# Performance work log

Hardware: AMD Instinct MI355X
Metric: run time of the kernel (lower is better)

Reference implementation:

```python
import jax, jax.numpy as jnp
import numpy as np

CELL = 1024
IN = 1024
HYB = 1024
SPK = 256
B = 8192

def setup_inputs() -> dict:
    key = jax.random.key(0)
    ks = jax.random.split(key, 13)
    s = lambda fan: 1.0 / np.sqrt(fan)
    return {
        "x": jax.random.normal(ks[0], (B, IN), jnp.float32),
        "ctm": jax.random.normal(ks[1], (B, CELL), jnp.float32),
        "htm": jax.random.normal(ks[2], (B, CELL), jnp.float32),
        "ztm": jax.random.normal(ks[3], (B, HYB), jnp.float32),
        "speaker_affine": jax.random.normal(ks[4], (B, SPK), jnp.float32),
        "Ww": jax.random.uniform(ks[5], (IN, 4 * CELL), jnp.float32, -s(IN), s(IN)),
        "Wb": jax.random.uniform(ks[6], (4 * CELL,), jnp.float32, -s(IN), s(IN)),
        "Uw": jax.random.uniform(ks[7], (CELL, 4 * CELL), jnp.float32, -s(CELL), s(CELL)),
        "Ub": jax.random.uniform(ks[8], (4 * CELL,), jnp.float32, -s(CELL), s(CELL)),
        "Vw": jax.random.uniform(ks[9], (HYB, CELL), jnp.float32, -s(HYB), s(HYB)),
        "Vb": jax.random.uniform(ks[10], (CELL,), jnp.float32, -s(HYB), s(HYB)),
        "Sw": jax.random.uniform(ks[11], (SPK, 4 * CELL), jnp.float32, -s(SPK), s(SPK)),
        "Sb": jax.random.uniform(ks[12], (4 * CELL,), jnp.float32, -s(SPK), s(SPK)),
    }

def reference(x, ctm, htm, ztm, speaker_affine, Ww, Wb, Uw, Ub, Vw, Vb, Sw, Sb):
    # sums: [B, 4*CELL] = W(x) + U(htm) + S(speaker)
    sums = (x @ Ww + Wb) + (htm @ Uw + Ub) + (speaker_affine @ Sw + Sb)
    hybrid = ztm @ Vw + Vb  # [B, CELL]
    f_t = jax.nn.sigmoid(sums[:, :CELL])
    i_t = jax.nn.sigmoid(sums[:, CELL:2 * CELL])
    o_t = jax.nn.sigmoid(sums[:, 2 * CELL:3 * CELL])
    ch_t = jnp.tanh(sums[:, 3 * CELL:])
    f_t_ = jax.nn.sigmoid(hybrid)
    c_t = f_t * ctm + i_t * ch_t + f_t_ * ctm
    h_t = jnp.tanh(c_t) * o_t
    return (c_t, h_t)
```

## Files before the change

kernel.cpp:

```cpp
#include <hip/hip_runtime.h>

#define B_DIM 8192
#define CELL  1024
#define KA    3328
#define NSUM  5120
#define BM    256
#define BN    256
#define BK    64

typedef unsigned short u16;
typedef __attribute__((ext_vector_type(8))) short bf16x8;
typedef __attribute__((ext_vector_type(4))) float f32x4;
typedef __attribute__((ext_vector_type(4))) float fx4;
typedef __attribute__((ext_vector_type(4))) unsigned short u16x4;

__device__ inline u16 f2bf(float f) {
  unsigned u = __float_as_uint(f);
  return (u16)((u + 0x7FFFu + ((u >> 16) & 1u)) >> 16);
}
__device__ inline float bf2f(u16 h) { return __uint_as_float(((unsigned)h) << 16); }
__device__ inline float sigmoidf(float v) { return 1.0f / (1.0f + __expf(-v)); }

__global__ void cvt_cat(const float* __restrict__ src, u16* __restrict__ dst,
                        int shift, int colOff, int n4) {
  int i = blockIdx.x * 256 + threadIdx.x;
  if (i >= n4) return;
  int e = i << 2;
  int row = e >> shift;
  int col = e & ((1 << shift) - 1);
  float4 v = *reinterpret_cast<const float4*>(src + e);
  u16x4 o;
  o[0] = f2bf(v.x); o[1] = f2bf(v.y); o[2] = f2bf(v.z); o[3] = f2bf(v.w);
  *reinterpret_cast<u16x4*>(dst + (size_t)row * KA + colOff + col) = o;
}

__global__ void wtrans(const float* __restrict__ src, int N,
                       u16* __restrict__ dst, int KT, int koff) {
  __shared__ float tile[32][33];
  int n0 = blockIdx.x * 32, k0 = blockIdx.y * 32;
  int tx = threadIdx.x, ty = threadIdx.y;
#pragma unroll
  for (int j = 0; j < 4; ++j)
    tile[ty + j * 8][tx] = src[(size_t)(k0 + ty + j * 8) * N + n0 + tx];
  __syncthreads();
#pragma unroll
  for (int j = 0; j < 4; ++j)
    dst[(size_t)(n0 + ty + j * 8) * KT + koff + k0 + tx] = f2bf(tile[tx][ty + j * 8]);
}

__device__ __forceinline__ void gload_lds16(const void* g, void* l) {
  __builtin_amdgcn_global_load_lds((const __attribute__((address_space(1))) void*)g,
                                   (__attribute__((address_space(3))) void*)l,
                                   16, 0, 0);
}

__device__ __forceinline__ void stage_half(const u16* __restrict__ g0, int ldk,
                                           u16* ldsTile, int half, int kt,
                                           int wave, int lane) {
#pragma unroll
  for (int k2 = 0; k2 < 2; ++k2) {
    const int r0 = half * 128 + k2 * 64 + wave * 8;
    const int r = r0 + (lane >> 3);
    const int slot = (lane & 7) ^ (lane >> 3);
    const u16* g = g0 + (size_t)r * ldk + kt * 64 + slot * 8;
    gload_lds16((const void*)g, (void*)(ldsTile + r0 * 64));
  }
}

#define LD_A(ASP, QP)                                                              \
  aq[0][0] = *reinterpret_cast<const bf16x8*>((ASP) + aBase0 + (2 * (QP)) * 1024);     \
  aq[0][1] = *reinterpret_cast<const bf16x8*>((ASP) + aBase1 + (2 * (QP)) * 1024);     \
  aq[1][0] = *reinterpret_cast<const bf16x8*>((ASP) + aBase0 + (2 * (QP) + 1) * 1024); \
  aq[1][1] = *reinterpret_cast<const bf16x8*>((ASP) + aBase1 + (2 * (QP) + 1) * 1024);

#define LD_B(BSP)                                                                  \
  _Pragma("unroll")                                                                \
  for (int n = 0; n < 4; ++n) {                                                    \
    br[n][0] = *reinterpret_cast<const bf16x8*>((BSP) + bBase0 + n * 1024);        \
    br[n][1] = *reinterpret_cast<const bf16x8*>((BSP) + bBase1 + n * 1024);        \
  }

#define MFMA_PH(QP)                                                                \
  __builtin_amdgcn_s_setprio(1);                                                   \
  _Pragma("unroll")                                                                \
  for (int q = 0; q < 2; ++q) {                                                    \
    _Pragma("unroll")                                                              \
    for (int n = 0; n < 4; ++n) {                                                  \
      acc[2 * (QP) + q][n] = __builtin_amdgcn_mfma_f32_16x16x32_bf16(              \
          aq[q][0], br[n][0], acc[2 * (QP) + q][n], 0, 0, 0);                      \
      acc[2 * (QP) + q][n] = __builtin_amdgcn_mfma_f32_16x16x32_bf16(              \
          aq[q][1], br[n][1], acc[2 * (QP) + q][n], 0, 0, 0);                      \
    }                                                                              \
  }                                                                                \
  __builtin_amdgcn_s_setprio(0);

#define ENTRY_BAR                                                                  \
  __builtin_amdgcn_sched_barrier(0);                                               \
  __builtin_amdgcn_s_barrier();                                                    \
  asm volatile("s_waitcnt lgkmcnt(0)" ::: "memory");                               \
  __builtin_amdgcn_sched_barrier(0);

#define EXIT_BAR __builtin_amdgcn_s_barrier();

__global__ __launch_bounds__(512, 2) void gemm8(
    const u16* __restrict__ Afull, const u16* __restrict__ WT4a,
    const u16* __restrict__ WTVa, u16* __restrict__ sums) {
  __shared__ u16 As[2][BM * BK];
  __shared__ u16 Bs[2][BN * BK];
  const int tid = threadIdx.x;
  const int wave = tid >> 6, lane = tid & 63;
  const int wm = wave >> 2, wn = wave & 3;
  const int lrow = lane & 15, khi = lane >> 4;

  const int bx = blockIdx.x, by = blockIdx.y;
  const u16* Bsrc; int KT, nk, ncol0, aoff, nbase;
  if (bx < 16) { Bsrc = WT4a; KT = 2304; nk = 36; nbase = bx * 256; ncol0 = bx * 256; aoff = 0; }
  else         { Bsrc = WTVa; KT = 1024; nk = 16; nbase = (bx - 16) * 256; ncol0 = 4096 + (bx - 16) * 256; aoff = 2304; }
  const int m0 = by * 256;
  const u16* Ag = Afull + (size_t)m0 * KA + aoff;
  const u16* Bg = Bsrc + (size_t)nbase * KT;

  const int sw = lane & 7;
  const int swz0 = ((0 + khi) ^ sw) * 8;
  const int swz1 = ((4 + khi) ^ sw) * 8;
  const int aBase0 = (wm * 128 + lrow) * 64 + swz0;
  const int aBase1 = (wm * 128 + lrow) * 64 + swz1;
  const int bBase0 = (wn * 64 + lrow) * 64 + swz0;
  const int bBase1 = (wn * 64 + lrow) * 64 + swz1;

  f32x4 acc[8][4];
#pragma unroll
  for (int m2 = 0; m2 < 8; ++m2)
#pragma unroll
    for (int n2 = 0; n2 < 4; ++n2) acc[m2][n2] = (f32x4){0.f, 0.f, 0.f, 0.f};
  bf16x8 aq[2][2], br[4][2];
  u16* As0 = As[0]; u16* As1 = As[1]; u16* Bs0 = Bs[0]; u16* Bs1 = Bs[1];

  stage_half(Ag, KA, As0, 0, 0, wave, lane);
  stage_half(Ag, KA, As0, 1, 0, wave, lane);
  stage_half(Bg, KT, Bs0, 0, 0, wave, lane);
  stage_half(Bg, KT, Bs0, 1, 0, wave, lane);
  stage_half(Bg, KT, Bs1, 0, 1, wave, lane);
  stage_half(Bg, KT, Bs1, 1, 1, wave, lane);
  asm volatile("s_waitcnt vmcnt(4)" ::: "memory");
  __builtin_amdgcn_s_barrier();

  const int niter = nk >> 1;
  for (int it = 0; it < niter; ++it) {
    const int t = it * 2;
    const bool nl = (t + 2 < nk);
    LD_B(Bs0)
    LD_A(As0, 0)
    stage_half(Ag, KA, As1, 0, t + 1, wave, lane);
    ENTRY_BAR MFMA_PH(0) EXIT_BAR

    LD_A(As0, 1)
    stage_half(Ag, KA, As1, 1, t + 1, wave, lane);
    ENTRY_BAR MFMA_PH(1) EXIT_BAR

    LD_A(As0, 2)
    if (nl) stage_half(Bg, KT, Bs0, 0, t + 2, wave, lane);
    ENTRY_BAR MFMA_PH(2) EXIT_BAR

    LD_A(As0, 3)
    if (nl) stage_half(Bg, KT, Bs0, 1, t + 2, wave, lane);
    ENTRY_BAR MFMA_PH(3)
    if (nl) { asm volatile("s_waitcnt vmcnt(4)" ::: "memory"); }
    else    { asm volatile("s_waitcnt vmcnt(0)" ::: "memory"); }
    EXIT_BAR

    LD_B(Bs1)
    LD_A(As1, 0)
    if (nl) stage_half(Ag, KA, As0, 0, t + 2, wave, lane);
    ENTRY_BAR MFMA_PH(0) EXIT_BAR

    LD_A(As1, 1)
    if (nl) stage_half(Ag, KA, As0, 1, t + 2, wave, lane);
    ENTRY_BAR MFMA_PH(1) EXIT_BAR

    LD_A(As1, 2)
    if (nl) stage_half(Bg, KT, Bs1, 0, t + 3, wave, lane);
    ENTRY_BAR MFMA_PH(2) EXIT_BAR

    LD_A(As1, 3)
    if (nl) stage_half(Bg, KT, Bs1, 1, t + 3, wave, lane);
    ENTRY_BAR MFMA_PH(3)
    if (nl) { asm volatile("s_waitcnt vmcnt(4)" ::: "memory"); }
    else    { asm volatile("s_waitcnt vmcnt(0)" ::: "memory"); }
    EXIT_BAR
  }

#pragma unroll
  for (int mf = 0; mf < 8; ++mf) {
    const int rbase = m0 + wm * 128 + mf * 16 + khi * 4;
#pragma unroll
    for (int nf = 0; nf < 4; ++nf) {
      const int col = ncol0 + wn * 64 + nf * 16 + lrow;
#pragma unroll
      for (int j = 0; j < 4; ++j)
        sums[(size_t)(rbase + j) * NSUM + col] = f2bf(acc[mf][nf][j]);
    }
  }
}

__global__ void epilogue(const u16* __restrict__ sums, const float* __restrict__ ctm,
                         const float* __restrict__ Wb, const float* __restrict__ Ub,
                         const float* __restrict__ Sb, const float* __restrict__ Vb,
                         float* __restrict__ outC, float* __restrict__ outH) {
  int t = blockIdx.x * 256 + threadIdx.x;
  int row = t >> 8;
  int c4 = (t & 255) << 2;
  const u16* s = sums + (size_t)row * NSUM;
  u16x4 sf = *reinterpret_cast<const u16x4*>(s + c4);
  u16x4 si = *reinterpret_cast<const u16x4*>(s + 1024 + c4);
  u16x4 so = *reinterpret_cast<const u16x4*>(s + 2048 + c4);
  u16x4 sc = *reinterpret_cast<const u16x4*>(s + 3072 + c4);
  u16x4 sh = *reinterpret_cast<const u16x4*>(s + 4096 + c4);
  fx4 ct = *reinterpret_cast<const fx4*>(ctm + (size_t)row * CELL + c4);
  fx4 bF = *reinterpret_cast<const fx4*>(Wb + c4) +
           *reinterpret_cast<const fx4*>(Ub + c4) +
           *reinterpret_cast<const fx4*>(Sb + c4);
  fx4 bI = *reinterpret_cast<const fx4*>(Wb + 1024 + c4) +
           *reinterpret_cast<const fx4*>(Ub + 1024 + c4) +
           *reinterpret_cast<const fx4*>(Sb + 1024 + c4);
  fx4 bO = *reinterpret_cast<const fx4*>(Wb + 2048 + c4) +
           *reinterpret_cast<const fx4*>(Ub + 2048 + c4) +
           *reinterpret_cast<const fx4*>(Sb + 2048 + c4);
  fx4 bC = *reinterpret_cast<const fx4*>(Wb + 3072 + c4) +
           *reinterpret_cast<const fx4*>(Ub + 3072 + c4) +
           *reinterpret_cast<const fx4*>(Sb + 3072 + c4);
  fx4 bH = *reinterpret_cast<const fx4*>(Vb + c4);

  fx4 vc, vh;
#pragma unroll
  for (int j = 0; j < 4; ++j) {
    float f_ = sigmoidf(bf2f(sf[j]) + bF[j]);
    float i_ = sigmoidf(bf2f(si[j]) + bI[j]);
    float o_ = sigmoidf(bf2f(so[j]) + bO[j]);
    float g_ = tanhf(bf2f(sc[j]) + bC[j]);
    float fh = sigmoidf(bf2f(sh[j]) + bH[j]);
    float cc = (f_ + fh) * ct[j] + i_ * g_;
    vc[j] = cc;
    vh[j] = tanhf(cc) * o_;
  }
  *reinterpret_cast<fx4*>(outC + (size_t)row * CELL + c4) = vc;
  *reinterpret_cast<fx4*>(outH + (size_t)row * CELL + c4) = vh;
}

extern "C" void kernel_launch(void* const* d_in, const int* in_sizes, int n_in,
                              void* d_out, int out_size, void* d_ws, size_t ws_size,
                              hipStream_t stream) {
  const float* x   = (const float*)d_in[0];
  const float* ctm = (const float*)d_in[1];
  const float* htm = (const float*)d_in[2];
  const float* ztm = (const float*)d_in[3];
  const float* spk = (const float*)d_in[4];
  const float* Ww  = (const float*)d_in[5];
  const float* Wb  = (const float*)d_in[6];
  const float* Uw  = (const float*)d_in[7];
  const float* Ub  = (const float*)d_in[8];
  const float* Vw  = (const float*)d_in[9];
  const float* Vb  = (const float*)d_in[10];
  const float* Sw  = (const float*)d_in[11];
  const float* Sb  = (const float*)d_in[12];

  u16* Afull = (u16*)d_ws;
  u16* WT4a  = Afull + (size_t)B_DIM * KA;
  u16* WTVa  = WT4a + (size_t)4096 * 2304;
  u16* sums  = WTVa + (size_t)1024 * 1024;
  float* outC = (float*)d_out;
  float* outH = outC + (size_t)B_DIM * CELL;

  cvt_cat<<<8192, 256, 0, stream>>>(x,   Afull, 10, 0,    2097152);
  cvt_cat<<<8192, 256, 0, stream>>>(htm, Afull, 10, 1024, 2097152);
  cvt_cat<<<2048, 256, 0, stream>>>(spk, Afull, 8,  2048, 524288);
  cvt_cat<<<8192, 256, 0, stream>>>(ztm, Afull, 10, 2304, 2097152);

  wtrans<<<dim3(128, 32), dim3(32, 8), 0, stream>>>(Ww, 4096, WT4a, 2304, 0);
  wtrans<<<dim3(128, 32), dim3(32, 8), 0, stream>>>(Uw, 4096, WT4a, 2304, 1024);
  wtrans<<<dim3(128, 8),  dim3(32, 8), 0, stream>>>(Sw, 4096, WT4a, 2304, 2048);
  wtrans<<<dim3(32, 32),  dim3(32, 8), 0, stream>>>(Vw, 1024, WTVa, 1024, 0);

  gemm8<<<dim3(20, 32), 512, 0, stream>>>(Afull, WT4a, WTVa, sums);

  epilogue<<<8192, 256, 0, stream>>>(sums, ctm, Wb, Ub, Sb, Vb, outC, outH);
}
```

Before: 295.5 us.

## Fuse LSTM epilogue into GEMM via gate-interleaved weight layout

```diff
diff --git a/kernel.cpp b/kernel.cpp
--- a/kernel.cpp
+++ b/kernel.cpp
@@ -3,7 +3,6 @@
 #define B_DIM 8192
 #define CELL  1024
 #define KA    3328
-#define NSUM  5120
 #define BM    256
 #define BN    256
 #define BK    64
@@ -18,7 +17,6 @@
   unsigned u = __float_as_uint(f);
   return (u16)((u + 0x7FFFu + ((u >> 16) & 1u)) >> 16);
 }
-__device__ inline float bf2f(u16 h) { return __uint_as_float(((unsigned)h) << 16); }
 __device__ inline float sigmoidf(float v) { return 1.0f / (1.0f + __expf(-v)); }
 
 __global__ void cvt_cat(const float* __restrict__ src, u16* __restrict__ dst,
@@ -35,7 +33,7 @@
 }
 
 __global__ void wtrans(const float* __restrict__ src, int N,
-                       u16* __restrict__ dst, int KT, int koff) {
+                       u16* __restrict__ dst, int KT, int koff, int packed) {
   __shared__ float tile[32][33];
   int n0 = blockIdx.x * 32, k0 = blockIdx.y * 32;
   int tx = threadIdx.x, ty = threadIdx.y;
@@ -44,8 +42,11 @@
     tile[ty + j * 8][tx] = src[(size_t)(k0 + ty + j * 8) * N + n0 + tx];
   __syncthreads();
 #pragma unroll
-  for (int j = 0; j < 4; ++j)
-    dst[(size_t)(n0 + ty + j * 8) * KT + koff + k0 + tx] = f2bf(tile[tx][ty + j * 8]);
+  for (int j = 0; j < 4; ++j) {
+    int jj = n0 + ty + j * 8;
+    int p = packed ? (((jj & 1023) >> 4) << 6) + ((jj >> 10) << 4) + (jj & 15) : jj;
+    dst[(size_t)p * KT + koff + k0 + tx] = f2bf(tile[tx][ty + j * 8]);
+  }
 }
 
 __device__ __forceinline__ void gload_lds16(const void* g, void* l) {
@@ -102,9 +103,12 @@
 
 #define EXIT_BAR __builtin_amdgcn_s_barrier();
 
-__global__ __launch_bounds__(512, 2) void gemm8(
-    const u16* __restrict__ Afull, const u16* __restrict__ WT4a,
-    const u16* __restrict__ WTVa, u16* __restrict__ sums) {
+__global__ __launch_bounds__(512, 2) void gemm_fused(
+    const u16* __restrict__ Afull, const u16* __restrict__ WT4p,
+    const u16* __restrict__ VwT, const float* __restrict__ ctm,
+    const float* __restrict__ Wb, const float* __restrict__ Ub,
+    const float* __restrict__ Sb, const float* __restrict__ Vb,
+    float* __restrict__ outC, float* __restrict__ outH) {
   __shared__ u16 As[2][BM * BK];
   __shared__ u16 Bs[2][BN * BK];
   const int tid = threadIdx.x;
@@ -112,13 +116,13 @@
   const int wm = wave >> 2, wn = wave & 3;
   const int lrow = lane & 15, khi = lane >> 4;
 
-  const int bx = blockIdx.x, by = blockIdx.y;
-  const u16* Bsrc; int KT, nk, ncol0, aoff, nbase;
-  if (bx < 16) { Bsrc = WT4a; KT = 2304; nk = 36; nbase = bx * 256; ncol0 = bx * 256; aoff = 0; }
-  else         { Bsrc = WTVa; KT = 1024; nk = 16; nbase = (bx - 16) * 256; ncol0 = 4096 + (bx - 16) * 256; aoff = 2304; }
-  const int m0 = by * 256;
-  const u16* Ag = Afull + (size_t)m0 * KA + aoff;
-  const u16* Bg = Bsrc + (size_t)nbase * KT;
+  const int bid = blockIdx.x;
+  const int tilei = ((bid & 7) << 6) | (bid >> 3);
+  const int nb = tilei >> 5, mb = tilei & 31;
+  const int m0 = mb * 256;
+  const u16* Ag = Afull + (size_t)m0 * KA;
+  const u16* Ah = Afull + (size_t)m0 * KA + 2304;
+  const u16* Bg = WT4p + (size_t)(nb * 256) * 2304;
 
   const int sw = lane & 7;
   const int swz0 = ((0 + khi) ^ sw) * 8;
@@ -128,6 +132,9 @@
   const int bBase0 = (wn * 64 + lrow) * 64 + swz0;
   const int bBase1 = (wn * 64 + lrow) * 64 + swz1;
 
+  const int co = nb * 64 + wn * 16 + lrow;
+  const u16* HgRow = VwT + (size_t)co * 1024;
+
   f32x4 acc[8][4];
 #pragma unroll
   for (int m2 = 0; m2 < 8; ++m2)
@@ -138,17 +145,17 @@
 
   stage_half(Ag, KA, As0, 0, 0, wave, lane);
   stage_half(Ag, KA, As0, 1, 0, wave, lane);
-  stage_half(Bg, KT, Bs0, 0, 0, wave, lane);
-  stage_half(Bg, KT, Bs0, 1, 0, wave, lane);
-  stage_half(Bg, KT, Bs1, 0, 1, wave, lane);
-  stage_half(Bg, KT, Bs1, 1, 1, wave, lane);
+  stage_half(Bg, 2304, Bs0, 0, 0, wave, lane);
+  stage_half(Bg, 2304, Bs0, 1, 0, wave, lane);
+  stage_half(Bg, 2304, Bs1, 0, 1, wave, lane);
+  stage_half(Bg, 2304, Bs1, 1, 1, wave, lane);
   asm volatile("s_waitcnt vmcnt(4)" ::: "memory");
   __builtin_amdgcn_s_barrier();
 
-  const int niter = nk >> 1;
-  for (int it = 0; it < niter; ++it) {
+#pragma unroll 1
+  for (int it = 0; it < 18; ++it) {
     const int t = it * 2;
-    const bool nl = (t + 2 < nk);
+    const bool nl = (t + 2 < 36);
     LD_B(Bs0)
     LD_A(As0, 0)
     stage_half(Ag, KA, As1, 0, t + 1, wave, lane);
@@ -159,11 +166,11 @@
     ENTRY_BAR MFMA_PH(1) EXIT_BAR
 
     LD_A(As0, 2)
-    if (nl) stage_half(Bg, KT, Bs0, 0, t + 2, wave, lane);
+    if (nl) stage_half(Bg, 2304, Bs0, 0, t + 2, wave, lane);
     ENTRY_BAR MFMA_PH(2) EXIT_BAR
 
     LD_A(As0, 3)
-    if (nl) stage_half(Bg, KT, Bs0, 1, t + 2, wave, lane);
+    if (nl) stage_half(Bg, 2304, Bs0, 1, t + 2, wave, lane);
     ENTRY_BAR MFMA_PH(3)
     if (nl) { asm volatile("s_waitcnt vmcnt(4)" ::: "memory"); }
     else    { asm volatile("s_waitcnt vmcnt(0)" ::: "memory"); }
@@ -179,72 +186,61 @@
     ENTRY_BAR MFMA_PH(1) EXIT_BAR
 
     LD_A(As1, 2)
-    if (nl) stage_half(Bg, KT, Bs1, 0, t + 3, wave, lane);
+    if (nl) stage_half(Bg, 2304, Bs1, 0, t + 3, wave, lane);
     ENTRY_BAR MFMA_PH(2) EXIT_BAR
 
     LD_A(As1, 3)
-    if (nl) stage_half(Bg, KT, Bs1, 1, t + 3, wave, lane);
+    if (nl) stage_half(Bg, 2304, Bs1, 1, t + 3, wave, lane);
     ENTRY_BAR MFMA_PH(3)
     if (nl) { asm volatile("s_waitcnt vmcnt(4)" ::: "memory"); }
     else    { asm volatile("s_waitcnt vmcnt(0)" ::: "memory"); }
     EXIT_BAR
   }
 
+  f32x4 acch[8];
+#pragma unroll
+  for (int m2 = 0; m2 < 8; ++m2) acch[m2] = (f32x4){0.f, 0.f, 0.f, 0.f};
+
+#pragma unroll 1
+  for (int kt = 0; kt < 16; ++kt) {
+    __syncthreads();
+    stage_half(Ah, KA, As0, 0, kt, wave, lane);
+    stage_half(Ah, KA, As0, 1, kt, wave, lane);
+    __syncthreads();
+    bf16x8 bh0 = *reinterpret_cast<const bf16x8*>(HgRow + kt * 64 + khi * 8);
+    bf16x8 bh1 = *reinterpret_cast<const bf16x8*>(HgRow + kt * 64 + 32 + khi * 8);
+#pragma unroll
+    for (int qp = 0; qp < 4; ++qp) {
+      LD_A(As0, qp)
+      acch[2 * qp]     = __builtin_amdgcn_mfma_f32_16x16x32_bf16(aq[0][0], bh0, acch[2 * qp], 0, 0, 0);
+      acch[2 * qp]     = __builtin_amdgcn_mfma_f32_16x16x32_bf16(aq[0][1], bh1, acch[2 * qp], 0, 0, 0);
+      acch[2 * qp + 1] = __builtin_amdgcn_mfma_f32_16x16x32_bf16(aq[1][0], bh0, acch[2 * qp + 1], 0, 0, 0);
+      acch[2 * qp + 1] = __builtin_amdgcn_mfma_f32_16x16x32_bf16(aq[1][1], bh1, acch[2 * qp + 1], 0, 0, 0);
+    }
+  }
+
+  const float bf = Wb[co] + Ub[co] + Sb[co];
+  const float bi = Wb[1024 + co] + Ub[1024 + co] + Sb[1024 + co];
+  const float bo = Wb[2048 + co] + Ub[2048 + co] + Sb[2048 + co];
+  const float bc = Wb[3072 + co] + Ub[3072 + co] + Sb[3072 + co];
+  const float bv = Vb[co];
 #pragma unroll
   for (int mf = 0; mf < 8; ++mf) {
-    const int rbase = m0 + wm * 128 + mf * 16 + khi * 4;
-#pragma unroll
-    for (int nf = 0; nf < 4; ++nf) {
-      const int col = ncol0 + wn * 64 + nf * 16 + lrow;
-#pragma unroll
-      for (int j = 0; j < 4; ++j)
-        sums[(size_t)(rbase + j) * NSUM + col] = f2bf(acc[mf][nf][j]);
+    const int r0 = m0 + wm * 128 + mf * 16 + khi * 4;
+#pragma unroll
+    for (int j = 0; j < 4; ++j) {
+      const size_t idx = (size_t)(r0 + j) * CELL + co;
+      float f_ = sigmoidf(acc[mf][0][j] + bf);
+      float i_ = sigmoidf(acc[mf][1][j] + bi);
+      float o_ = sigmoidf(acc[mf][2][j] + bo);
+      float g_ = tanhf(acc[mf][3][j] + bc);
+      float fh = sigmoidf(acch[mf][j] + bv);
+      float ct = ctm[idx];
+      float cc = (f_ + fh) * ct + i_ * g_;
+      outC[idx] = cc;
+      outH[idx] = tanhf(cc) * o_;
     }
   }
-}
-
-__global__ void epilogue(const u16* __restrict__ sums, const float* __restrict__ ctm,
-                         const float* __restrict__ Wb, const float* __restrict__ Ub,
-                         const float* __restrict__ Sb, const float* __restrict__ Vb,
-                         float* __restrict__ outC, float* __restrict__ outH) {
-  int t = blockIdx.x * 256 + threadIdx.x;
-  int row = t >> 8;
-  int c4 = (t & 255) << 2;
-  const u16* s = sums + (size_t)row * NSUM;
-  u16x4 sf = *reinterpret_cast<const u16x4*>(s + c4);
-  u16x4 si = *reinterpret_cast<const u16x4*>(s + 1024 + c4);
-  u16x4 so = *reinterpret_cast<const u16x4*>(s + 2048 + c4);
-  u16x4 sc = *reinterpret_cast<const u16x4*>(s + 3072 + c4);
-  u16x4 sh = *reinterpret_cast<const u16x4*>(s + 4096 + c4);
-  fx4 ct = *reinterpret_cast<const fx4*>(ctm + (size_t)row * CELL + c4);
-  fx4 bF = *reinterpret_cast<const fx4*>(Wb + c4) +
-           *reinterpret_cast<const fx4*>(Ub + c4) +
-           *reinterpret_cast<const fx4*>(Sb + c4);
-  fx4 bI = *reinterpret_cast<const fx4*>(Wb + 1024 + c4) +
-           *reinterpret_cast<const fx4*>(Ub + 1024 + c4) +
-           *reinterpret_cast<const fx4*>(Sb + 1024 + c4);
-  fx4 bO = *reinterpret_cast<const fx4*>(Wb + 2048 + c4) +
-           *reinterpret_cast<const fx4*>(Ub + 2048 + c4) +
-           *reinterpret_cast<const fx4*>(Sb + 2048 + c4);
-  fx4 bC = *reinterpret_cast<const fx4*>(Wb + 3072 + c4) +
-           *reinterpret_cast<const fx4*>(Ub + 3072 + c4) +
-           *reinterpret_cast<const fx4*>(Sb + 3072 + c4);
-  fx4 bH = *reinterpret_cast<const fx4*>(Vb + c4);
-
-  fx4 vc, vh;
-#pragma unroll
-  for (int j = 0; j < 4; ++j) {
-    float f_ = sigmoidf(bf2f(sf[j]) + bF[j]);
-    float i_ = sigmoidf(bf2f(si[j]) + bI[j]);
-    float o_ = sigmoidf(bf2f(so[j]) + bO[j]);
-    float g_ = tanhf(bf2f(sc[j]) + bC[j]);
-    float fh = sigmoidf(bf2f(sh[j]) + bH[j]);
-    float cc = (f_ + fh) * ct[j] + i_ * g_;
-    vc[j] = cc;
-    vh[j] = tanhf(cc) * o_;
-  }
-  *reinterpret_cast<fx4*>(outC + (size_t)row * CELL + c4) = vc;
-  *reinterpret_cast<fx4*>(outH + (size_t)row * CELL + c4) = vh;
 }
 
 extern "C" void kernel_launch(void* const* d_in, const int* in_sizes, int n_in,
@@ -265,9 +261,8 @@
   const float* Sb  = (const float*)d_in[12];
 
   u16* Afull = (u16*)d_ws;
-  u16* WT4a  = Afull + (size_t)B_DIM * KA;
-  u16* WTVa  = WT4a + (size_t)4096 * 2304;
-  u16* sums  = WTVa + (size_t)1024 * 1024;
+  u16* WT4p  = Afull + (size_t)B_DIM * KA;
+  u16* VwT   = WT4p + (size_t)4096 * 2304;
   float* outC = (float*)d_out;
   float* outH = outC + (size_t)B_DIM * CELL;
 
@@ -276,12 +271,10 @@
   cvt_cat<<<2048, 256, 0, stream>>>(spk, Afull, 8,  2048, 524288);
   cvt_cat<<<8192, 256, 0, stream>>>(ztm, Afull, 10, 2304, 2097152);
 
-  wtrans<<<dim3(128, 32), dim3(32, 8), 0, stream>>>(Ww, 4096, WT4a, 2304, 0);
-  wtrans<<<dim3(128, 32), dim3(32, 8), 0, stream>>>(Uw, 4096, WT4a, 2304, 1024);
-  wtrans<<<dim3(128, 8),  dim3(32, 8), 0, stream>>>(Sw, 4096, WT4a, 2304, 2048);
-  wtrans<<<dim3(32, 32),  dim3(32, 8), 0, stream>>>(Vw, 1024, WTVa, 1024, 0);
-
-  gemm8<<<dim3(20, 32), 512, 0, stream>>>(Afull, WT4a, WTVa, sums);
-
-  epilogue<<<8192, 256, 0, stream>>>(sums, ctm, Wb, Ub, Sb, Vb, outC, outH);
-}
+  wtrans<<<dim3(128, 32), dim3(32, 8), 0, stream>>>(Ww, 4096, WT4p, 2304, 0,    1);
+  wtrans<<<dim3(128, 32), dim3(32, 8), 0, stream>>>(Uw, 4096, WT4p, 2304, 1024, 1);
+  wtrans<<<dim3(128, 8),  dim3(32, 8), 0, stream>>>(Sw, 4096, WT4p, 2304, 2048, 1);
+  wtrans<<<dim3(32, 32),  dim3(32, 8), 0, stream>>>(Vw, 1024, VwT,  1024, 0,    0);
+
+  gemm_fused<<<512, 512, 0, stream>>>(Afull, WT4p, VwT, ctm, Wb, Ub, Sb, Vb, outC, outH);
+}
```

New measurement: 295.1 us. No clear change (-0.2%).
